# Performance work log

Hardware: AMD Instinct MI355X
Metric: run time of the kernel (lower is better)

The kernel has to match this reference:

```python
import jax, jax.numpy as jnp
import numpy as np

ALPHA, BETA, GAMMA = 1.0, 0.5, 0.3
EPS = 1e-08


def setup_inputs() -> dict:
    key = jax.random.key(0)
    k1, k2, k3, k4, k5 = jax.random.split(key, 5)
    B, C, F = 32, 256, 2048
    return {
        "mag_hat": jax.random.normal(k1, (B, C, F), dtype=jnp.float32),
        "phase_hat": jax.random.normal(k2, (B, C, F), dtype=jnp.float32),
        "mag_target": jax.random.normal(k3, (B, C, F), dtype=jnp.float32),
        "phase_target": jax.random.normal(k4, (B, C, F), dtype=jnp.float32),
        "pci_target": jax.random.uniform(k5, (B, C, C), dtype=jnp.float32),
    }


def _pci(phase):
    # phase: (B, C, F). Naive form is mean_f cos/sin(phi_i - phi_j) over a
    # (B,C,C,F) broadcast; rewrite with cos(a-b)=ca*cb+sa*sb and
    # sin(a-b)=sa*cb-ca*sb as two batched GEMMs on (C,F) matrices.
    c = jnp.cos(phase)
    s = jnp.sin(phase)
    inv_f = 1.0 / phase.shape[-1]
    real = (jnp.einsum('bif,bjf->bij', c, c) + jnp.einsum('bif,bjf->bij', s, s)) * inv_f
    imag = (jnp.einsum('bif,bjf->bij', s, c) - jnp.einsum('bif,bjf->bij', c, s)) * inv_f
    return jnp.sqrt(real * real + imag * imag + EPS)


def reference(mag_hat, phase_hat, mag_target, phase_target, pci_target):
    mag_loss = jnp.mean((mag_hat - mag_target) ** 2)
    phase_loss = jnp.mean(1.0 - jnp.cos(phase_hat - phase_target))
    pci_hat = _pci(phase_hat)
    coh_loss = jnp.mean((pci_hat - pci_target) ** 2)
    total = ALPHA * mag_loss + BETA * phase_loss + GAMMA * coh_loss
    return (total, mag_loss, phase_loss, coh_loss)
```

## Files before the change

### kernel.cpp

```cpp
#include <hip/hip_runtime.h>
#include <hip/hip_bf16.h>

#define ALPHA_ 1.0f
#define BETA_  0.5f
#define GAMMA_ 0.3f
#define EPS_   1e-8f

typedef unsigned short u16;
typedef unsigned int u32;

constexpr int B_ = 32, C_ = 256, F_ = 2048;
constexpr int NTOT = B_ * C_ * F_;
constexpr int G8   = NTOT / 8;
constexpr int NCC  = B_ * C_ * C_;

typedef __bf16 bf16x8 __attribute__((ext_vector_type(8)));
typedef float  f32x4  __attribute__((ext_vector_type(4)));

__device__ __forceinline__ u32 f2bf(float x) {
    unsigned u = __float_as_uint(x);
    u += 0x7fffu + ((u >> 16) & 1u);
    return (u >> 16);
}

__device__ __forceinline__ void async_copy16(const void* g, void* l) {
    __builtin_amdgcn_global_load_lds(
        (const __attribute__((address_space(1))) unsigned int*)g,
        (__attribute__((address_space(3))) unsigned int*)l,
        16, 0, 0);
}

__device__ __forceinline__ void ew_body(int g,
    float4 p0, float4 p1, float4 q0, float4 q1,
    float4 a0, float4 a1, float4 b0, float4 b1,
    float& msum, float& psum, int4* __restrict__ cb4, int4* __restrict__ sb4)
{
    float pv[8] = {p0.x, p0.y, p0.z, p0.w, p1.x, p1.y, p1.z, p1.w};
    float qv[8] = {q0.x, q0.y, q0.z, q0.w, q1.x, q1.y, q1.z, q1.w};
    float av[8] = {a0.x, a0.y, a0.z, a0.w, a1.x, a1.y, a1.z, a1.w};
    float bv[8] = {b0.x, b0.y, b0.z, b0.w, b1.x, b1.y, b1.z, b1.w};
    u32 cu[8], su[8];
    #pragma unroll
    for (int j = 0; j < 8; j++) {
        float dm = av[j] - bv[j];
        msum += dm * dm;
        psum += 1.f - __cosf(pv[j] - qv[j]);
        float s, c;
        __sincosf(pv[j], &s, &c);
        cu[j] = f2bf(c);
        su[j] = f2bf(s);
    }
    cb4[g] = make_int4((int)(cu[0] | (cu[1] << 16)), (int)(cu[2] | (cu[3] << 16)),
                       (int)(cu[4] | (cu[5] << 16)), (int)(cu[6] | (cu[7] << 16)));
    sb4[g] = make_int4((int)(su[0] | (su[1] << 16)), (int)(su[2] | (su[3] << 16)),
                       (int)(su[4] | (su[5] << 16)), (int)(su[6] | (su[7] << 16)));
}

__global__ void __launch_bounds__(256)
ew_kernel(const float4* __restrict__ mh, const float4* __restrict__ ph,
          const float4* __restrict__ mt, const float4* __restrict__ pt,
          int4* __restrict__ cb4, int4* __restrict__ sb4,
          float* __restrict__ accum)
{
    __shared__ float sm[4], sp[4];
    const int tid    = blockIdx.x * 256 + threadIdx.x;
    const int stride = 2048 * 256;
    float msum = 0.f, psum = 0.f;

    #pragma unroll
    for (int half = 0; half < 2; ++half) {
        int g0 = tid + (2 * half) * stride;
        int g1 = g0 + stride;
        float4 p00 = ph[2*g0], p01 = ph[2*g0+1];
        float4 q00 = pt[2*g0], q01 = pt[2*g0+1];
        float4 a00 = mh[2*g0], a01 = mh[2*g0+1];
        float4 b00 = mt[2*g0], b01 = mt[2*g0+1];
        float4 p10 = ph[2*g1], p11 = ph[2*g1+1];
        float4 q10 = pt[2*g1], q11 = pt[2*g1+1];
        float4 a10 = mh[2*g1], a11 = mh[2*g1+1];
        float4 b10 = mt[2*g1], b11 = mt[2*g1+1];
        ew_body(g0, p00, p01, q00, q01, a00, a01, b00, b01, msum, psum, cb4, sb4);
        ew_body(g1, p10, p11, q10, q11, a10, a11, b10, b11, msum, psum, cb4, sb4);
    }

    #pragma unroll
    for (int o = 32; o > 0; o >>= 1) {
        msum += __shfl_down(msum, o, 64);
        psum += __shfl_down(psum, o, 64);
    }
    int lane = threadIdx.x & 63, wv = threadIdx.x >> 6;
    if (lane == 0) { sm[wv] = msum; sp[wv] = psum; }
    __syncthreads();
    if (threadIdx.x == 0) {
        atomicAdd(&accum[0], sm[0] + sm[1] + sm[2] + sm[3]);
        atomicAdd(&accum[1], sp[0] + sp[1] + sp[2] + sp[3]);
    }
}

__global__ void __launch_bounds__(256)
pci_kernel(const u16* __restrict__ cb, const u16* __restrict__ sb,
           const float* __restrict__ tgt, float* __restrict__ accum)
{
    __shared__ char lds[32768];
    __shared__ float sred[4];
    char* la = lds;
    char* lb = lds + 16384;

    const int g  = blockIdx.x;
    const int x  = g & 7, sq = g >> 3;
    const int y  = (x << 2) | (sq & 3);
    const int tt = sq >> 2;
    const int i0 = (tt >> 2) * 64, j0 = (tt & 3) * 64;

    const int t    = threadIdx.x;
    const int lane = t & 63, w = t >> 6;
    const int wrow = (w >> 1) * 32, wcol = (w & 1) * 32;
    const int m = lane & 15, q = lane >> 4;

    const char* gA[4];
    const char* gB[4];
    {
        const int p = lane & 15;
        #pragma unroll
        for (int r = 0; r < 4; ++r) {
            int row = w * 16 + r * 4 + (lane >> 4);
            int c   = p ^ (row & 15);
            const u16* arr = (c < 8) ? cb : sb;
            int cc = c & 7;
            gA[r] = (const char*)arr + ((size_t)(y * 256 + i0 + row)) * 4096 + cc * 16;
            gB[r] = (const char*)arr + ((size_t)(y * 256 + j0 + row)) * 4096 + cc * 16;
        }
    }

    f32x4 zero = {0.f, 0.f, 0.f, 0.f};
    f32x4 accR[2][2], accSC[2][2], accCS[2][2];
    #pragma unroll
    for (int a = 0; a < 2; a++)
        #pragma unroll
        for (int c = 0; c < 2; c++) {
            accR[a][c] = zero; accSC[a][c] = zero; accCS[a][c] = zero;
        }

    for (int it = 0; it < 32; ++it) {
        __syncthreads();
        #pragma unroll
        for (int r = 0; r < 4; ++r) {
            async_copy16(gA[r], la + w * 4096 + r * 1024);
            async_copy16(gB[r], lb + w * 4096 + r * 1024);
            gA[r] += 128; gB[r] += 128;
        }
        __syncthreads();

        #pragma unroll
        for (int s = 0; s < 2; ++s) {
            bf16x8 fac[2], fas[2], fbc[2], fbs[2];
            #pragma unroll
            for (int a = 0; a < 2; a++) {
                const char* base = la + (wrow + a * 16 + m) * 256;
                int pc = ((4 * s + q) ^ m) * 16;
                fac[a] = *(const bf16x8*)(base + pc);
                fas[a] = *(const bf16x8*)(base + (pc ^ 128));
            }
            #pragma unroll
            for (int c = 0; c < 2; c++) {
                const char* base = lb + (wcol + c * 16 + m) * 256;
                int pc = ((4 * s + q) ^ m) * 16;
                fbc[c] = *(const bf16x8*)(base + pc);
                fbs[c] = *(const bf16x8*)(base + (pc ^ 128));
            }
            #pragma unroll
            for (int a = 0; a < 2; a++)
                #pragma unroll
                for (int c = 0; c < 2; c++) {
                    accR[a][c]  = __builtin_amdgcn_mfma_f32_16x16x32_bf16(fac[a], fbc[c], accR[a][c], 0, 0, 0);
                    accR[a][c]  = __builtin_amdgcn_mfma_f32_16x16x32_bf16(fas[a], fbs[c], accR[a][c], 0, 0, 0);
                    accSC[a][c] = __builtin_amdgcn_mfma_f32_16x16x32_bf16(fas[a], fbc[c], accSC[a][c], 0, 0, 0);
                    accCS[a][c] = __builtin_amdgcn_mfma_f32_16x16x32_bf16(fac[a], fbs[c], accCS[a][c], 0, 0, 0);
                }
        }
    }

    const float inv_f = 1.0f / (float)F_;
    float coh = 0.f;
    const float* tb = tgt + (size_t)y * (C_ * C_);
    #pragma unroll
    for (int a = 0; a < 2; a++)
        #pragma unroll
        for (int c = 0; c < 2; c++) {
            int irow = i0 + wrow + a * 16 + q * 4;
            int jcol = j0 + wcol + c * 16 + m;
            #pragma unroll
            for (int r = 0; r < 4; r++) {
                float re = accR[a][c][r] * inv_f;
                float im = (accSC[a][c][r] - accCS[a][c][r]) * inv_f;
                float p  = sqrtf(re * re + im * im + EPS_);
                float d  = p - tb[(irow + r) * C_ + jcol];
                coh += d * d;
            }
        }

    #pragma unroll
    for (int o = 32; o > 0; o >>= 1) coh += __shfl_down(coh, o, 64);
    if (lane == 0) sred[w] = coh;
    __syncthreads();
    if (t == 0) atomicAdd(&accum[2], sred[0] + sred[1] + sred[2] + sred[3]);
}

__global__ void fin_kernel(const float* __restrict__ accum, float* __restrict__ out)
{
    if (threadIdx.x == 0) {
        float mag = accum[0] * (1.0f / (float)NTOT);
        float phs = accum[1] * (1.0f / (float)NTOT);
        float coh = accum[2] * (1.0f / (float)NCC);
        out[0] = ALPHA_ * mag + BETA_ * phs + GAMMA_ * coh;
        out[1] = mag;
        out[2] = phs;
        out[3] = coh;
    }
}

extern "C" void kernel_launch(void* const* d_in, const int* in_sizes, int n_in,
                              void* d_out, int out_size, void* d_ws, size_t ws_size,
                              hipStream_t stream)
{
    const float* mh  = (const float*)d_in[0];
    const float* ph  = (const float*)d_in[1];
    const float* mt  = (const float*)d_in[2];
    const float* pt  = (const float*)d_in[3];
    const float* tgt = (const float*)d_in[4];
    float* out = (float*)d_out;

    float* accum = (float*)d_ws;
    u16* cb = (u16*)((char*)d_ws + 256);
    u16* sb = cb + (size_t)NTOT;

    hipMemsetAsync(d_ws, 0, 16, stream);

    ew_kernel<<<2048, 256, 0, stream>>>(
        (const float4*)mh, (const float4*)ph, (const float4*)mt, (const float4*)pt,
        (int4*)cb, (int4*)sb, accum);

    pci_kernel<<<512, 256, 0, stream>>>(cb, sb, tgt, accum);

    fin_kernel<<<1, 64, 0, stream>>>(accum, out);
}
```

Baseline: 309.8 us.

## Exploit PCI symmetry to compute only upper-triangular tiles, split elementwise kernel

The PCI magnitude matrix is symmetric, so the coherence kernel now computes only the 10 upper-triangular 64x64 tiles per batch instead of all 16. Each off-diagonal result is compared against both target entries (i,j) and (j,i). Diagonal tiles reuse the A tile in LDS rather than loading B a second time. The elementwise kernel is also split into separate magnitude and phase kernels. That adds one launch and changes the load/compute mix, with the aim of cutting GEMM work by about 37%.

```diff
diff --git a/kernel.cpp b/kernel.cpp
--- a/kernel.cpp
+++ b/kernel.cpp
@@ -30,71 +30,71 @@
         16, 0, 0);
 }
 
-__device__ __forceinline__ void ew_body(int g,
-    float4 p0, float4 p1, float4 q0, float4 q1,
-    float4 a0, float4 a1, float4 b0, float4 b1,
-    float& msum, float& psum, int4* __restrict__ cb4, int4* __restrict__ sb4)
-{
-    float pv[8] = {p0.x, p0.y, p0.z, p0.w, p1.x, p1.y, p1.z, p1.w};
-    float qv[8] = {q0.x, q0.y, q0.z, q0.w, q1.x, q1.y, q1.z, q1.w};
-    float av[8] = {a0.x, a0.y, a0.z, a0.w, a1.x, a1.y, a1.z, a1.w};
-    float bv[8] = {b0.x, b0.y, b0.z, b0.w, b1.x, b1.y, b1.z, b1.w};
-    u32 cu[8], su[8];
-    #pragma unroll
-    for (int j = 0; j < 8; j++) {
-        float dm = av[j] - bv[j];
-        msum += dm * dm;
-        psum += 1.f - __cosf(pv[j] - qv[j]);
-        float s, c;
-        __sincosf(pv[j], &s, &c);
-        cu[j] = f2bf(c);
-        su[j] = f2bf(s);
-    }
-    cb4[g] = make_int4((int)(cu[0] | (cu[1] << 16)), (int)(cu[2] | (cu[3] << 16)),
-                       (int)(cu[4] | (cu[5] << 16)), (int)(cu[6] | (cu[7] << 16)));
-    sb4[g] = make_int4((int)(su[0] | (su[1] << 16)), (int)(su[2] | (su[3] << 16)),
-                       (int)(su[4] | (su[5] << 16)), (int)(su[6] | (su[7] << 16)));
-}
-
 __global__ void __launch_bounds__(256)
-ew_kernel(const float4* __restrict__ mh, const float4* __restrict__ ph,
-          const float4* __restrict__ mt, const float4* __restrict__ pt,
-          int4* __restrict__ cb4, int4* __restrict__ sb4,
-          float* __restrict__ accum)
-{
-    __shared__ float sm[4], sp[4];
+mag_kernel(const float4* __restrict__ mh, const float4* __restrict__ mt,
+           float* __restrict__ accum)
+{
+    __shared__ float sm[4];
     const int tid    = blockIdx.x * 256 + threadIdx.x;
-    const int stride = 2048 * 256;
-    float msum = 0.f, psum = 0.f;
-
-    #pragma unroll
-    for (int half = 0; half < 2; ++half) {
-        int g0 = tid + (2 * half) * stride;
-        int g1 = g0 + stride;
-        float4 p00 = ph[2*g0], p01 = ph[2*g0+1];
-        float4 q00 = pt[2*g0], q01 = pt[2*g0+1];
-        float4 a00 = mh[2*g0], a01 = mh[2*g0+1];
-        float4 b00 = mt[2*g0], b01 = mt[2*g0+1];
-        float4 p10 = ph[2*g1], p11 = ph[2*g1+1];
-        float4 q10 = pt[2*g1], q11 = pt[2*g1+1];
-        float4 a10 = mh[2*g1], a11 = mh[2*g1+1];
-        float4 b10 = mt[2*g1], b11 = mt[2*g1+1];
-        ew_body(g0, p00, p01, q00, q01, a00, a01, b00, b01, msum, psum, cb4, sb4);
-        ew_body(g1, p10, p11, q10, q11, a10, a11, b10, b11, msum, psum, cb4, sb4);
-    }
-
-    #pragma unroll
-    for (int o = 32; o > 0; o >>= 1) {
-        msum += __shfl_down(msum, o, 64);
-        psum += __shfl_down(psum, o, 64);
-    }
+    const int stride = 4096 * 256;
+    float msum = 0.f;
+
+    #pragma unroll
+    for (int it = 0; it < 2; ++it) {
+        int g = tid + it * stride;
+        float4 a0 = mh[2*g], a1 = mh[2*g+1];
+        float4 b0 = mt[2*g], b1 = mt[2*g+1];
+        float d0 = a0.x-b0.x, d1 = a0.y-b0.y, d2 = a0.z-b0.z, d3 = a0.w-b0.w;
+        float d4 = a1.x-b1.x, d5 = a1.y-b1.y, d6 = a1.z-b1.z, d7 = a1.w-b1.w;
+        msum += d0*d0 + d1*d1 + d2*d2 + d3*d3 + d4*d4 + d5*d5 + d6*d6 + d7*d7;
+    }
+
+    #pragma unroll
+    for (int o = 32; o > 0; o >>= 1) msum += __shfl_down(msum, o, 64);
     int lane = threadIdx.x & 63, wv = threadIdx.x >> 6;
-    if (lane == 0) { sm[wv] = msum; sp[wv] = psum; }
+    if (lane == 0) sm[wv] = msum;
     __syncthreads();
-    if (threadIdx.x == 0) {
-        atomicAdd(&accum[0], sm[0] + sm[1] + sm[2] + sm[3]);
-        atomicAdd(&accum[1], sp[0] + sp[1] + sp[2] + sp[3]);
-    }
+    if (threadIdx.x == 0) atomicAdd(&accum[0], sm[0] + sm[1] + sm[2] + sm[3]);
+}
+
+__global__ void __launch_bounds__(256)
+phase_kernel(const float4* __restrict__ ph, const float4* __restrict__ pt,
+             int4* __restrict__ cb4, int4* __restrict__ sb4,
+             float* __restrict__ accum)
+{
+    __shared__ float sp[4];
+    const int tid    = blockIdx.x * 256 + threadIdx.x;
+    const int stride = 4096 * 256;
+    float psum = 0.f;
+
+    #pragma unroll
+    for (int it = 0; it < 2; ++it) {
+        int g = tid + it * stride;
+        float4 p0 = ph[2*g], p1 = ph[2*g+1];
+        float4 q0 = pt[2*g], q1 = pt[2*g+1];
+        float pv[8] = {p0.x, p0.y, p0.z, p0.w, p1.x, p1.y, p1.z, p1.w};
+        float qv[8] = {q0.x, q0.y, q0.z, q0.w, q1.x, q1.y, q1.z, q1.w};
+        u32 cu[8], su[8];
+        #pragma unroll
+        for (int j = 0; j < 8; j++) {
+            psum += 1.f - __cosf(pv[j] - qv[j]);
+            float s, c;
+            __sincosf(pv[j], &s, &c);
+            cu[j] = f2bf(c);
+            su[j] = f2bf(s);
+        }
+        cb4[g] = make_int4((int)(cu[0] | (cu[1] << 16)), (int)(cu[2] | (cu[3] << 16)),
+                           (int)(cu[4] | (cu[5] << 16)), (int)(cu[6] | (cu[7] << 16)));
+        sb4[g] = make_int4((int)(su[0] | (su[1] << 16)), (int)(su[2] | (su[3] << 16)),
+                           (int)(su[4] | (su[5] << 16)), (int)(su[6] | (su[7] << 16)));
+    }
+
+    #pragma unroll
+    for (int o = 32; o > 0; o >>= 1) psum += __shfl_down(psum, o, 64);
+    int lane = threadIdx.x & 63, wv = threadIdx.x >> 6;
+    if (lane == 0) sp[wv] = psum;
+    __syncthreads();
+    if (threadIdx.x == 0) atomicAdd(&accum[1], sp[0] + sp[1] + sp[2] + sp[3]);
 }
 
 __global__ void __launch_bounds__(256)
@@ -109,8 +109,14 @@
     const int g  = blockIdx.x;
     const int x  = g & 7, sq = g >> 3;
     const int y  = (x << 2) | (sq & 3);
-    const int tt = sq >> 2;
-    const int i0 = (tt >> 2) * 64, j0 = (tt & 3) * 64;
+    const int job = sq >> 2;
+    int ti, tj;
+    if      (job < 4) { ti = 0; tj = job; }
+    else if (job < 7) { ti = 1; tj = job - 3; }
+    else if (job < 9) { ti = 2; tj = job - 5; }
+    else              { ti = 3; tj = 3; }
+    const bool diag = (ti == tj);
+    const int i0 = ti * 64, j0 = tj * 64;
 
     const int t    = threadIdx.x;
     const int lane = t & 63, w = t >> 6;
@@ -131,6 +137,7 @@
             gB[r] = (const char*)arr + ((size_t)(y * 256 + j0 + row)) * 4096 + cc * 16;
         }
     }
+    char* lbp = diag ? la : lb;
 
     f32x4 zero = {0.f, 0.f, 0.f, 0.f};
     f32x4 accR[2][2], accSC[2][2], accCS[2][2];
@@ -146,8 +153,14 @@
         #pragma unroll
         for (int r = 0; r < 4; ++r) {
             async_copy16(gA[r], la + w * 4096 + r * 1024);
-            async_copy16(gB[r], lb + w * 4096 + r * 1024);
-            gA[r] += 128; gB[r] += 128;
+            gA[r] += 128;
+        }
+        if (!diag) {
+            #pragma unroll
+            for (int r = 0; r < 4; ++r) {
+                async_copy16(gB[r], lb + w * 4096 + r * 1024);
+                gB[r] += 128;
+            }
         }
         __syncthreads();
 
@@ -163,7 +176,7 @@
             }
             #pragma unroll
             for (int c = 0; c < 2; c++) {
-                const char* base = lb + (wcol + c * 16 + m) * 256;
+                const char* base = lbp + (wcol + c * 16 + m) * 256;
                 int pc = ((4 * s + q) ^ m) * 16;
                 fbc[c] = *(const bf16x8*)(base + pc);
                 fbs[c] = *(const bf16x8*)(base + (pc ^ 128));
@@ -187,15 +200,22 @@
     for (int a = 0; a < 2; a++)
         #pragma unroll
         for (int c = 0; c < 2; c++) {
-            int irow = i0 + wrow + a * 16 + q * 4;
+            int ir0  = i0 + wrow + a * 16 + q * 4;
             int jcol = j0 + wcol + c * 16 + m;
             #pragma unroll
             for (int r = 0; r < 4; r++) {
+                int irow = ir0 + r;
                 float re = accR[a][c][r] * inv_f;
                 float im = (accSC[a][c][r] - accCS[a][c][r]) * inv_f;
                 float p  = sqrtf(re * re + im * im + EPS_);
-                float d  = p - tb[(irow + r) * C_ + jcol];
-                coh += d * d;
+                float d1 = p - tb[irow * C_ + jcol];
+                float d2 = p - tb[jcol * C_ + irow];
+                if (diag) {
+                    if (jcol > irow)       coh += d1 * d1 + d2 * d2;
+                    else if (jcol == irow) coh += d1 * d1;
+                } else {
+                    coh += d1 * d1 + d2 * d2;
+                }
             }
         }
 
@@ -236,11 +256,13 @@
 
     hipMemsetAsync(d_ws, 0, 16, stream);
 
-    ew_kernel<<<2048, 256, 0, stream>>>(
-        (const float4*)mh, (const float4*)ph, (const float4*)mt, (const float4*)pt,
-        (int4*)cb, (int4*)sb, accum);
-
-    pci_kernel<<<512, 256, 0, stream>>>(cb, sb, tgt, accum);
+    mag_kernel<<<4096, 256, 0, stream>>>(
+        (const float4*)mh, (const float4*)mt, accum);
+
+    phase_kernel<<<4096, 256, 0, stream>>>(
+        (const float4*)ph, (const float4*)pt, (int4*)cb, (int4*)sb, accum);
+
+    pci_kernel<<<320, 256, 0, stream>>>(cb, sb, tgt, accum);
 
     fin_kernel<<<1, 64, 0, stream>>>(accum, out);
 }
```

Measured after the change: 316.5 us. 2.1% more time.
